# Optimization experiments

Measured on AMD Instinct MI355X. Metric: run time of the kernel, lower is better.

The kernel has to match this reference:

```python
import jax, jax.numpy as jnp
import numpy as np

B, N, M, C, H = 4, 1024, 1024, 768, 12
HD = C // H          # head_dim = in_dim // num_heads = 64
D = H * HD           # inner dim = 768
HID = int(4.0 * C)   # mlp hidden = 3072
EPS = 1e-6
SCALE = HD ** -0.5


def _lin(k, out_d, in_d):
    return jax.random.normal(k, (out_d, in_d), jnp.float32) * 0.02


def setup_inputs() -> dict:
    key = jax.random.key(0)
    ks = jax.random.split(key, 20)
    p = {
        "x": jax.random.normal(ks[0], (B, N, C), jnp.float32),
        "src": jax.random.normal(ks[1], (B, M, C), jnp.float32),
        # self-attention (x stream)
        "w_qkv": _lin(ks[2], 3 * D, C), "w_proj": _lin(ks[3], C, D), "b_proj": jnp.zeros((C,), jnp.float32),
        # self-attention (src stream)
        "w_qkv_s": _lin(ks[4], 3 * D, C), "w_proj_s": _lin(ks[5], C, D), "b_proj_s": jnp.zeros((C,), jnp.float32),
        # bidirectional cross-attention
        "w_qk": _lin(ks[6], 2 * D, C), "w_qk_src": _lin(ks[7], 2 * D, C),
        "w_v": _lin(ks[8], D, C), "w_v_src": _lin(ks[9], D, C),
        "w_cp": _lin(ks[10], C, D), "b_cp": jnp.zeros((C,), jnp.float32),
        "w_cp_src": _lin(ks[11], C, D), "b_cp_src": jnp.zeros((C,), jnp.float32),
        # MLPs
        "mlp1_w": _lin(ks[12], HID, C), "mlp1_b": jnp.zeros((HID,), jnp.float32),
        "mlp2_w": _lin(ks[13], C, HID), "mlp2_b": jnp.zeros((C,), jnp.float32),
        "mlp1s_w": _lin(ks[14], HID, C), "mlp1s_b": jnp.zeros((HID,), jnp.float32),
        "mlp2s_w": _lin(ks[15], C, HID), "mlp2s_b": jnp.zeros((C,), jnp.float32),
    }
    for name in ["ln1", "ln1s", "lnc", "lncs", "ln2", "ln2s"]:
        p[name + "_w"] = jnp.ones((C,), jnp.float32)
        p[name + "_b"] = jnp.zeros((C,), jnp.float32)
    return p


def _ln(x, w, b):
    mu = x.mean(-1, keepdims=True)
    var = ((x - mu) ** 2).mean(-1, keepdims=True)
    return (x - mu) * jax.lax.rsqrt(var + EPS) * w + b


def _heads(t):  # [B,T,(H d)] -> [B,H,T,d]
    b, t_, hd = t.shape
    return t.reshape(b, t_, H, hd // H).transpose(0, 2, 1, 3)


def _merge(t):  # [B,H,T,d] -> [B,T,(H d)]
    b, h, t_, d = t.shape
    return t.transpose(0, 2, 1, 3).reshape(b, t_, h * d)


def _self_attn(x, w_qkv, w_p, b_p):
    b, n, _ = x.shape
    qkv = (x @ w_qkv.T).reshape(b, n, 3, H, HD)
    q = qkv[:, :, 0].transpose(0, 2, 1, 3) * SCALE  # [B,H,N,hd]
    k = qkv[:, :, 1].transpose(0, 2, 1, 3)
    v = qkv[:, :, 2].transpose(0, 2, 1, 3)
    attn = jax.nn.softmax(jnp.einsum('bhnd,bhmd->bhnm', q, k), axis=-1)
    o = _merge(jnp.einsum('bhnm,bhmd->bhnd', attn, v))
    return o @ w_p.T + b_p


def _cross_attn(x, src, w_qk, w_qk_src, w_v, w_v_src, w_cp, b_cp, w_cp_src, b_cp_src):
    # rearrange 'b n (h d) -> b h n d' with h=H on the 2D-wide qk output
    # puts [q_h | k_h] of width 2*HD in the last axis per head
    qk = _heads(x @ w_qk.T)            # [B,H,N,2*hd]
    qk_s = _heads(src @ w_qk_src.T)    # [B,H,M,2*hd]
    v = _heads(x @ w_v.T)              # [B,H,N,hd]
    v_s = _heads(src @ w_v_src.T)      # [B,H,M,hd]
    q, kx = qk[..., :HD] * SCALE, qk[..., HD:] * SCALE
    q_s, k_s = qk_s[..., :HD], qk_s[..., HD:]
    attn = jax.nn.softmax(jnp.einsum('bhnd,bhmd->bhnm', q, q_s), axis=-1)      # x attends to src
    attn_s = jax.nn.softmax(jnp.einsum('bhnd,bhmd->bhmn', kx, k_s), axis=-1)   # src attends to x
    y = _merge(jnp.einsum('bhnm,bhmd->bhnd', attn, v_s)) @ w_cp.T + b_cp
    y_s = _merge(jnp.einsum('bhmn,bhnd->bhmd', attn_s, v)) @ w_cp_src.T + b_cp_src
    return y, y_s


def _mlp(x, w1, b1, w2, b2):
    return jax.nn.gelu(x @ w1.T + b1, approximate=False) @ w2.T + b2


def reference(x, src,
              w_qkv, w_proj, b_proj, w_qkv_s, w_proj_s, b_proj_s,
              w_qk, w_qk_src, w_v, w_v_src, w_cp, b_cp, w_cp_src, b_cp_src,
              mlp1_w, mlp1_b, mlp2_w, mlp2_b, mlp1s_w, mlp1s_b, mlp2s_w, mlp2s_b,
              ln1_w, ln1_b, ln1s_w, ln1s_b, lnc_w, lnc_b, lncs_w, lncs_b,
              ln2_w, ln2_b, ln2s_w, ln2s_b):
    # per-stream self attention (eval: dropout/drop_path identity, no layerscale)
    x = x + _self_attn(_ln(x, ln1_w, ln1_b), w_qkv, w_proj, b_proj)
    src = src + _self_attn(_ln(src, ln1s_w, ln1s_b), w_qkv_s, w_proj_s, b_proj_s)
    # bidirectional cross attention
    y, y_s = _cross_attn(_ln(x, lnc_w, lnc_b), _ln(src, lncs_w, lncs_b),
                         w_qk, w_qk_src, w_v, w_v_src, w_cp, b_cp, w_cp_src, b_cp_src)
    x = x + y
    src = src + y_s
    # per-stream MLP
    x = x + _mlp(_ln(x, ln2_w, ln2_b), mlp1_w, mlp1_b, mlp2_w, mlp2_b)
    src = src + _mlp(_ln(src, ln2s_w, ln2s_b), mlp1s_w, mlp1s_b, mlp2s_w, mlp2s_b)
    return (x, src)
```

## Files before the change

### kernel.cpp

```cpp
#include <hip/hip_runtime.h>
#include <hip/hip_bf16.h>
#include <cmath>


typedef __bf16 bf16_t;
typedef __attribute__((ext_vector_type(8))) __bf16 bf16x8;
typedef __attribute__((ext_vector_type(4))) __bf16 bf16x4;
typedef __attribute__((ext_vector_type(4))) float f32x4;

#define NTOK 4096
#define SCALE_ATTN 0.125f

__device__ __forceinline__ void gload16(const void* g, void* l) {
    __builtin_amdgcn_global_load_lds((const __attribute__((address_space(1))) void*)g,
                                     (__attribute__((address_space(3))) void*)l, 16, 0, 0);
}

struct CvtTab {
    const float* src[14];
    bf16_t* dst[14];
    int n[14];
};
__global__ __launch_bounds__(256) void cvt_all_kernel(CvtTab t) {
    int seg = blockIdx.y;
    int base = blockIdx.x * 2048 + threadIdx.x * 8;
    if (base >= t.n[seg]) return;
    const float* s = t.src[seg];
    float4 a = *(const float4*)(s + base);
    float4 b = *(const float4*)(s + base + 4);
    bf16x8 o;
    o[0] = (bf16_t)a.x; o[1] = (bf16_t)a.y; o[2] = (bf16_t)a.z; o[3] = (bf16_t)a.w;
    o[4] = (bf16_t)b.x; o[5] = (bf16_t)b.y; o[6] = (bf16_t)b.z; o[7] = (bf16_t)b.w;
    *(bf16x8*)(t.dst[seg] + base) = o;
}

__global__ __launch_bounds__(256) void ln_kernel(const float* __restrict__ X,
                                                 const float* __restrict__ w,
                                                 const float* __restrict__ b,
                                                 bf16_t* __restrict__ out) {
    int row = blockIdx.x, t = threadIdx.x;
    const float* x = X + (size_t)row * 768;
    float v0 = x[t], v1 = x[t + 256], v2 = x[t + 512];
    float s = v0 + v1 + v2;
    float s2 = v0 * v0 + v1 * v1 + v2 * v2;
#pragma unroll
    for (int off = 32; off > 0; off >>= 1) {
        s += __shfl_down(s, off);
        s2 += __shfl_down(s2, off);
    }
    __shared__ float as_[4], as2_[4];
    int wave = t >> 6;
    if ((t & 63) == 0) { as_[wave] = s; as2_[wave] = s2; }
    __syncthreads();
    float tot = as_[0] + as_[1] + as_[2] + as_[3];
    float tot2 = as2_[0] + as2_[1] + as2_[2] + as2_[3];
    float mu = tot * (1.f / 768.f);
    float var = tot2 * (1.f / 768.f) - mu * mu;
    float rstd = rsqrtf(var + 1e-6f);
    bf16_t* o = out + (size_t)row * 768;
    o[t]       = (bf16_t)((v0 - mu) * rstd * w[t]       + b[t]);
    o[t + 256] = (bf16_t)((v1 - mu) * rstd * w[t + 256] + b[t + 256]);
    o[t + 512] = (bf16_t)((v2 - mu) * rstd * w[t + 512] + b[t + 512]);
}

__global__ __launch_bounds__(256, 3) void gemm_qkv_kernel(const bf16_t* __restrict__ A,
                                                          const bf16_t* __restrict__ W,
                                                          bf16_t* __restrict__ outQK,
                                                          bf16_t* __restrict__ outVT) {
    __shared__ bf16_t Alds[128 * 64];
    __shared__ bf16_t Blds[128 * 64];
    const int K = 768, GX = 18;
    const int tid = threadIdx.x;
    const int f = blockIdx.x + GX * blockIdx.y;
    const int slot = f >> 3;
    const int bm = (f & 7) * 4 + slot / GX, bn = slot % GX;
    const int lane = tid & 63, wid = tid >> 6;
    const int wm = wid >> 1, wn = wid & 1;
    const int l15 = lane & 15, lh = lane >> 4;
    f32x4 acc[4][4] = {};

    const int lr = lane >> 3;
    const int lc = ((lane & 7) ^ lr) * 8;
    const bf16_t* gA = A + (size_t)(bm * 128 + lr) * K + lc;
    const bf16_t* gB = W + (size_t)(bn * 128 + lr) * K + lc;

    for (int k0 = 0; k0 < K; k0 += 64) {
        __syncthreads();
#pragma unroll
        for (int q = 0; q < 4; ++q) {
            int r0 = (wid * 4 + q) * 8;
            gload16(gA + (size_t)r0 * K + k0, &Alds[r0 * 64]);
            gload16(gB + (size_t)r0 * K + k0, &Blds[r0 * 64]);
        }
        __syncthreads();
#pragma unroll
        for (int kk = 0; kk < 2; ++kk) {
            bf16x8 av[4], bv[4];
#pragma unroll
            for (int i = 0; i < 4; ++i) {
                int rA = wm * 64 + i * 16 + l15;
                int cc = kk * 4 + lh;
                av[i] = *(const bf16x8*)&Alds[rA * 64 + ((cc ^ (rA & 7)) * 8)];
                int rB = wn * 64 + i * 16 + l15;
                bv[i] = *(const bf16x8*)&Blds[rB * 64 + ((cc ^ (rB & 7)) * 8)];
            }
#pragma unroll
            for (int i = 0; i < 4; ++i)
#pragma unroll
                for (int j = 0; j < 4; ++j)
                    acc[i][j] = __builtin_amdgcn_mfma_f32_16x16x32_bf16(av[i], bv[j], acc[i][j], 0, 0, 0);
        }
    }
#pragma unroll
    for (int i = 0; i < 4; ++i) {
        int row0 = bm * 128 + wm * 64 + i * 16 + lh * 4;
#pragma unroll
        for (int j = 0; j < 4; ++j) {
            int col = bn * 128 + wn * 64 + j * 16 + l15;
            if (col < 1536) {
#pragma unroll
                for (int p = 0; p < 4; ++p)
                    outQK[(size_t)(row0 + p) * 1536 + col] = (bf16_t)acc[i][j][p];
            } else {
                bf16x4 pk;
#pragma unroll
                for (int p = 0; p < 4; ++p) pk[p] = (bf16_t)acc[i][j][p];
                *(bf16x4*)&outVT[(size_t)(col - 1536) * NTOK + row0] = pk;
            }
        }
    }
}

__global__ __launch_bounds__(256, 3) void gemm_gelu_kernel(const bf16_t* __restrict__ A,
                                                           const bf16_t* __restrict__ W,
                                                           const float* __restrict__ bias,
                                                           bf16_t* __restrict__ outB) {
    __shared__ bf16_t Alds[128 * 64];
    __shared__ bf16_t Blds[128 * 64];
    const int K = 768, N = 3072, GX = 24;
    const int tid = threadIdx.x;
    const int f = blockIdx.x + GX * blockIdx.y;
    const int slot = f >> 3;
    const int bm = (f & 7) * 4 + slot / GX, bn = slot % GX;
    const int lane = tid & 63, wid = tid >> 6;
    const int wm = wid >> 1, wn = wid & 1;
    const int l15 = lane & 15, lh = lane >> 4;
    f32x4 acc[4][4] = {};

    const int lr = lane >> 3;
    const int lc = ((lane & 7) ^ lr) * 8;
    const bf16_t* gA = A + (size_t)(bm * 128 + lr) * K + lc;
    const bf16_t* gB = W + (size_t)(bn * 128 + lr) * K + lc;

    for (int k0 = 0; k0 < K; k0 += 64) {
        __syncthreads();
#pragma unroll
        for (int q = 0; q < 4; ++q) {
            int r0 = (wid * 4 + q) * 8;
            gload16(gA + (size_t)r0 * K + k0, &Alds[r0 * 64]);
            gload16(gB + (size_t)r0 * K + k0, &Blds[r0 * 64]);
        }
        __syncthreads();
#pragma unroll
        for (int kk = 0; kk < 2; ++kk) {
            bf16x8 av[4], bv[4];
#pragma unroll
            for (int i = 0; i < 4; ++i) {
                int rA = wm * 64 + i * 16 + l15;
                int cc = kk * 4 + lh;
                av[i] = *(const bf16x8*)&Alds[rA * 64 + ((cc ^ (rA & 7)) * 8)];
                int rB = wn * 64 + i * 16 + l15;
                bv[i] = *(const bf16x8*)&Blds[rB * 64 + ((cc ^ (rB & 7)) * 8)];
            }
#pragma unroll
            for (int i = 0; i < 4; ++i)
#pragma unroll
                for (int j = 0; j < 4; ++j)
                    acc[i][j] = __builtin_amdgcn_mfma_f32_16x16x32_bf16(av[i], bv[j], acc[i][j], 0, 0, 0);
        }
    }
#pragma unroll
    for (int i = 0; i < 4; ++i) {
        int row0 = bm * 128 + wm * 64 + i * 16 + lh * 4;
#pragma unroll
        for (int j = 0; j < 4; ++j) {
            int col = bn * 128 + wn * 64 + j * 16 + l15;
            float bv_ = bias[col];
#pragma unroll
            for (int p = 0; p < 4; ++p) {
                float v = acc[i][j][p] + bv_;
                v = 0.5f * v * (1.f + erff(v * 0.70710678118654752f));
                outB[(size_t)(row0 + p) * N + col] = (bf16_t)v;
            }
        }
    }
}

__global__ __launch_bounds__(256, 4) void gemm64_kernel(const bf16_t* __restrict__ A,
                                                        const bf16_t* __restrict__ W,
                                                        const float* __restrict__ bias,
                                                        const float* __restrict__ res,
                                                        float* __restrict__ outF,
                                                        int K) {
    __shared__ bf16_t Alds[128 * 64];
    __shared__ bf16_t Blds[64 * 64];
    const int N = 768, GX = 12;
    const int tid = threadIdx.x;
    const int f = blockIdx.x + GX * blockIdx.y;
    const int slot = f >> 3;
    const int bm = (f & 7) * 4 + slot / GX, bn = slot % GX;
    const int lane = tid & 63, wid = tid >> 6;
    const int l15 = lane & 15, lh = lane >> 4;
    f32x4 acc[2][4] = {};

    const int lr = lane >> 3;
    const int lc = ((lane & 7) ^ lr) * 8;
    const bf16_t* gA = A + (size_t)(bm * 128 + lr) * K + lc;
    const bf16_t* gB = W + (size_t)(bn * 64 + lr) * K + lc;

    for (int k0 = 0; k0 < K; k0 += 64) {
        __syncthreads();
#pragma unroll
        for (int q = 0; q < 4; ++q) {
            int r0 = (wid * 4 + q) * 8;
            gload16(gA + (size_t)r0 * K + k0, &Alds[r0 * 64]);
        }
#pragma unroll
        for (int q = 0; q < 2; ++q) {
            int r0 = (wid * 2 + q) * 8;
            gload16(gB + (size_t)r0 * K + k0, &Blds[r0 * 64]);
        }
        __syncthreads();
#pragma unroll
        for (int kk = 0; kk < 2; ++kk) {
            bf16x8 av[2], bv[4];
#pragma unroll
            for (int i = 0; i < 2; ++i) {
                int rA = wid * 32 + i * 16 + l15;
                int cc = kk * 4 + lh;
                av[i] = *(const bf16x8*)&Alds[rA * 64 + ((cc ^ (rA & 7)) * 8)];
            }
#pragma unroll
            for (int j = 0; j < 4; ++j) {
                int rB = j * 16 + l15;
                int cc = kk * 4 + lh;
                bv[j] = *(const bf16x8*)&Blds[rB * 64 + ((cc ^ (rB & 7)) * 8)];
            }
#pragma unroll
            for (int i = 0; i < 2; ++i)
#pragma unroll
                for (int j = 0; j < 4; ++j)
                    acc[i][j] = __builtin_amdgcn_mfma_f32_16x16x32_bf16(av[i], bv[j], acc[i][j], 0, 0, 0);
        }
    }
#pragma unroll
    for (int i = 0; i < 2; ++i) {
        int row0 = bm * 128 + wid * 32 + i * 16 + lh * 4;
#pragma unroll
        for (int j = 0; j < 4; ++j) {
            int col = bn * 64 + j * 16 + l15;
            float bv_ = bias[col];
#pragma unroll
            for (int p = 0; p < 4; ++p) {
                size_t idx = (size_t)(row0 + p) * N + col;
                outF[idx] = acc[i][j][p] + bv_ + res[idx];
            }
        }
    }
}

__global__ __launch_bounds__(256, 3) void attn_mfma_kernel(const bf16_t* __restrict__ Qp,
                                                           const bf16_t* __restrict__ Kp,
                                                           const bf16_t* __restrict__ VTp,
                                                           bf16_t* __restrict__ Op,
                                                           int ldQ, int ldK,
                                                           int hsQ, int hsK,
                                                           float scale) {
    __shared__ bf16_t Kl[2][64 * 64];
    __shared__ bf16_t Vl[2][64 * 64];
    __shared__ bf16_t Pl[4][16 * 64];
    const int tid = threadIdx.x, lane = tid & 63, w = tid >> 6;
    const int l15 = lane & 15, lh = lane >> 4;
    const int f = blockIdx.x + (blockIdx.y << 4);
    const int slot = f >> 3;
    const int bh = (f & 7) * 6 + (slot >> 4);
    const int q0 = (slot & 15) * 64;
    const int b = bh / 12, h = bh % 12;

    const bf16_t* qptr = Qp + (size_t)(b * 1024 + q0 + w * 16 + l15) * ldQ + h * hsQ + lh * 8;
    bf16x8 qf0 = *(const bf16x8*)qptr;
    bf16x8 qf1 = *(const bf16x8*)(qptr + 32);

    f32x4 oacc[4] = {};
    float m_run[4], l_run[4];
#pragma unroll
    for (int p = 0; p < 4; ++p) { m_run[p] = -1e30f; l_run[p] = 0.f; }

    const int lr = lane >> 3;
    const int lc = ((lane & 7) ^ lr) * 8;
    const bf16_t* kbase = Kp + (size_t)(b * 1024 + lr) * ldK + h * hsK + lc;
    const bf16_t* vbase = VTp + (size_t)(h * 64 + lr) * NTOK + b * 1024 + lc;

    auto stage = [&](int bb, int kt) {
#pragma unroll
        for (int q = 0; q < 2; ++q) {
            int r0 = (w * 2 + q) * 8;
            gload16(kbase + (size_t)(kt + r0) * ldK, &Kl[bb][r0 * 64]);
            gload16(vbase + (size_t)r0 * NTOK + kt, &Vl[bb][r0 * 64]);
        }
    };

    stage(0, 0);
    __syncthreads();

    for (int it = 0; it < 16; ++it) {
        const int cur = it & 1;
        if (it < 15) stage(cur ^ 1, (it + 1) * 64);

        f32x4 s[4] = {};
#pragma unroll
        for (int t = 0; t < 4; ++t) {
            int key = t * 16 + l15;
            bf16x8 kf0 = *(const bf16x8*)&Kl[cur][key * 64 + ((lh ^ (key & 7)) * 8)];
            bf16x8 kf1 = *(const bf16x8*)&Kl[cur][key * 64 + (((4 + lh) ^ (key & 7)) * 8)];
            s[t] = __builtin_amdgcn_mfma_f32_16x16x32_bf16(qf0, kf0, s[t], 0, 0, 0);
            s[t] = __builtin_amdgcn_mfma_f32_16x16x32_bf16(qf1, kf1, s[t], 0, 0, 0);
        }

#pragma unroll
        for (int p = 0; p < 4; ++p) {
            float v0 = s[0][p] * scale, v1 = s[1][p] * scale;
            float v2 = s[2][p] * scale, v3 = s[3][p] * scale;
            float mloc = fmaxf(fmaxf(v0, v1), fmaxf(v2, v3));
#pragma unroll
            for (int off = 1; off < 16; off <<= 1) mloc = fmaxf(mloc, __shfl_xor(mloc, off));
            float mnew = fmaxf(m_run[p], mloc);
            float corr = __expf(m_run[p] - mnew);
            float p0 = __expf(v0 - mnew), p1 = __expf(v1 - mnew);
            float p2 = __expf(v2 - mnew), p3 = __expf(v3 - mnew);
            float ps = p0 + p1 + p2 + p3;
#pragma unroll
            for (int off = 1; off < 16; off <<= 1) ps += __shfl_xor(ps, off);
            l_run[p] = l_run[p] * corr + ps;
            m_run[p] = mnew;
            oacc[0][p] *= corr; oacc[1][p] *= corr; oacc[2][p] *= corr; oacc[3][p] *= corr;
            int r = lh * 4 + p;
            bf16_t* pr = &Pl[w][r * 64];
            int cb = l15 >> 3, ce = l15 & 7, rs = r & 7;
            pr[((0 + cb) ^ rs) * 8 + ce] = (bf16_t)p0;
            pr[((2 + cb) ^ rs) * 8 + ce] = (bf16_t)p1;
            pr[((4 + cb) ^ rs) * 8 + ce] = (bf16_t)p2;
            pr[((6 + cb) ^ rs) * 8 + ce] = (bf16_t)p3;
        }

#pragma unroll
        for (int kk = 0; kk < 2; ++kk) {
            bf16x8 pf = *(const bf16x8*)&Pl[w][l15 * 64 + (((kk * 4 + lh) ^ (l15 & 7)) * 8)];
#pragma unroll
            for (int dt = 0; dt < 4; ++dt) {
                int d = dt * 16 + l15;
                bf16x8 vf = *(const bf16x8*)&Vl[cur][d * 64 + (((kk * 4 + lh) ^ (d & 7)) * 8)];
                oacc[dt] = __builtin_amdgcn_mfma_f32_16x16x32_bf16(pf, vf, oacc[dt], 0, 0, 0);
            }
        }

        __syncthreads();
    }

    float inv[4];
#pragma unroll
    for (int p = 0; p < 4; ++p) inv[p] = 1.f / l_run[p];
#pragma unroll
    for (int dt = 0; dt < 4; ++dt) {
#pragma unroll
        for (int p = 0; p < 4; ++p) {
            int row = q0 + w * 16 + lh * 4 + p;
            int col = h * 64 + dt * 16 + l15;
            Op[(size_t)(b * 1024 + row) * 768 + col] = (bf16_t)(oacc[dt][p] * inv[p]);
        }
    }
}

extern "C" void kernel_launch(void* const* d_in, const int* in_sizes, int n_in,
                              void* d_out, int out_size, void* d_ws, size_t ws_size,
                              hipStream_t stream) {
    const float* x_in   = (const float*)d_in[0];
    const float* src_in = (const float*)d_in[1];
    const float* b_proj   = (const float*)d_in[4];
    const float* b_proj_s = (const float*)d_in[7];
    const float* b_cp     = (const float*)d_in[13];
    const float* b_cp_s   = (const float*)d_in[15];
    const float* mlp1_b   = (const float*)d_in[17];
    const float* mlp2_b   = (const float*)d_in[19];
    const float* mlp1s_b  = (const float*)d_in[21];
    const float* mlp2s_b  = (const float*)d_in[23];
    const float* ln1_w  = (const float*)d_in[24];
    const float* ln1_b  = (const float*)d_in[25];
    const float* ln1s_w = (const float*)d_in[26];
    const float* ln1s_b = (const float*)d_in[27];
    const float* lnc_w  = (const float*)d_in[28];
    const float* lnc_b  = (const float*)d_in[29];
    const float* lncs_w = (const float*)d_in[30];
    const float* lncs_b = (const float*)d_in[31];
    const float* ln2_w  = (const float*)d_in[32];
    const float* ln2_b  = (const float*)d_in[33];
    const float* ln2s_w = (const float*)d_in[34];
    const float* ln2s_b = (const float*)d_in[35];

    char* ws = (char*)d_ws;
    size_t off = 0;
    auto alloc = [&](size_t bytes) -> void* {
        void* p = ws + off;
        off = (off + bytes + 255) & ~(size_t)255;
        return p;
    };

    bf16_t* bw_qkv_x = (bf16_t*)alloc((size_t)2304 * 768 * 2);
    bf16_t* bw_proj_x = (bf16_t*)alloc((size_t)768 * 768 * 2);
    bf16_t* bw_qkv_s = (bf16_t*)alloc((size_t)2304 * 768 * 2);
    bf16_t* bw_proj_s = (bf16_t*)alloc((size_t)768 * 768 * 2);
    bf16_t* bw_cx    = (bf16_t*)alloc((size_t)2304 * 768 * 2);
    bf16_t* bw_cs    = (bf16_t*)alloc((size_t)2304 * 768 * 2);
    bf16_t* bw_cp    = (bf16_t*)alloc((size_t)768 * 768 * 2);
    bf16_t* bw_cp_s  = (bf16_t*)alloc((size_t)768 * 768 * 2);
    bf16_t* bw_mlp1  = (bf16_t*)alloc((size_t)3072 * 768 * 2);
    bf16_t* bw_mlp2  = (bf16_t*)alloc((size_t)768 * 3072 * 2);
    bf16_t* bw_mlp1s = (bf16_t*)alloc((size_t)3072 * 768 * 2);
    bf16_t* bw_mlp2s = (bf16_t*)alloc((size_t)768 * 3072 * 2);

    bf16_t* arena = (bf16_t*)alloc((size_t)NTOK * 3072 * 2 * 2);
    bf16_t* LN_A = (bf16_t*)alloc((size_t)NTOK * 768 * 2);
    bf16_t* LN_B = (bf16_t*)alloc((size_t)NTOK * 768 * 2);
    bf16_t* O_A  = (bf16_t*)alloc((size_t)NTOK * 768 * 2);
    bf16_t* O_B  = (bf16_t*)alloc((size_t)NTOK * 768 * 2);

    float* Xst = (float*)d_out;
    float* Sst = (float*)d_out + (size_t)NTOK * 768;

    bf16_t* SQK = arena;
    bf16_t* VTs = arena + (size_t)NTOK * 1536;
    bf16_t* QKx = arena;
    bf16_t* QKs = arena + (size_t)NTOK * 1536;
    bf16_t* VxT = arena + (size_t)NTOK * 3072;
    bf16_t* VsT = arena + (size_t)NTOK * 3072 + (size_t)768 * NTOK;
    bf16_t* H_A = arena;
    bf16_t* H_B = arena + (size_t)NTOK * 3072;

    CvtTab tab;
    const float* csrc[14] = {(const float*)d_in[2], (const float*)d_in[3],
                             (const float*)d_in[5], (const float*)d_in[6],
                             (const float*)d_in[8], (const float*)d_in[10],
                             (const float*)d_in[9], (const float*)d_in[11],
                             (const float*)d_in[12], (const float*)d_in[14],
                             (const float*)d_in[16], (const float*)d_in[18],
                             (const float*)d_in[20], (const float*)d_in[22]};
    bf16_t* cdst[14] = {bw_qkv_x, bw_proj_x, bw_qkv_s, bw_proj_s,
                        bw_cx, bw_cx + (size_t)1536 * 768,
                        bw_cs, bw_cs + (size_t)1536 * 768,
                        bw_cp, bw_cp_s, bw_mlp1, bw_mlp2, bw_mlp1s, bw_mlp2s};
    int cn[14] = {2304 * 768, 768 * 768, 2304 * 768, 768 * 768,
                  1536 * 768, 768 * 768, 1536 * 768, 768 * 768,
                  768 * 768, 768 * 768, 3072 * 768, 768 * 3072, 3072 * 768, 768 * 3072};
    for (int i = 0; i < 14; ++i) { tab.src[i] = csrc[i]; tab.dst[i] = cdst[i]; tab.n[i] = cn[i]; }
    cvt_all_kernel<<<dim3(1152, 14), 256, 0, stream>>>(tab);

    const dim3 blk(256);
    const dim3 qkv_grid(18, 32);
    const dim3 g64_grid(12, 32);
    const dim3 gelu_grid(24, 32);
    const dim3 attn_grid(16, 48);

    ln_kernel<<<NTOK, blk, 0, stream>>>(x_in, ln1_w, ln1_b, LN_A);
    gemm_qkv_kernel<<<qkv_grid, blk, 0, stream>>>(LN_A, bw_qkv_x, SQK, VTs);
    attn_mfma_kernel<<<attn_grid, blk, 0, stream>>>(SQK, SQK + 768, VTs, O_A, 1536, 1536, 64, 64, SCALE_ATTN);
    gemm64_kernel<<<g64_grid, blk, 0, stream>>>(O_A, bw_proj_x, b_proj, x_in, Xst, 768);

    ln_kernel<<<NTOK, blk, 0, stream>>>(src_in, ln1s_w, ln1s_b, LN_A);
    gemm_qkv_kernel<<<qkv_grid, blk, 0, stream>>>(LN_A, bw_qkv_s, SQK, VTs);
    attn_mfma_kernel<<<attn_grid, blk, 0, stream>>>(SQK, SQK + 768, VTs, O_A, 1536, 1536, 64, 64, SCALE_ATTN);
    gemm64_kernel<<<g64_grid, blk, 0, stream>>>(O_A, bw_proj_s, b_proj_s, src_in, Sst, 768);

    ln_kernel<<<NTOK, blk, 0, stream>>>(Xst, lnc_w, lnc_b, LN_A);
    ln_kernel<<<NTOK, blk, 0, stream>>>(Sst, lncs_w, lncs_b, LN_B);
    gemm_qkv_kernel<<<qkv_grid, blk, 0, stream>>>(LN_A, bw_cx, QKx, VxT);
    gemm_qkv_kernel<<<qkv_grid, blk, 0, stream>>>(LN_B, bw_cs, QKs, VsT);
    attn_mfma_kernel<<<attn_grid, blk, 0, stream>>>(QKx, QKs, VsT, O_A, 1536, 1536, 128, 128, SCALE_ATTN);
    attn_mfma_kernel<<<attn_grid, blk, 0, stream>>>(QKs + 64, QKx + 64, VxT, O_B, 1536, 1536, 128, 128, SCALE_ATTN);
    gemm64_kernel<<<g64_grid, blk, 0, stream>>>(O_A, bw_cp, b_cp, Xst, Xst, 768);
    gemm64_kernel<<<g64_grid, blk, 0, stream>>>(O_B, bw_cp_s, b_cp_s, Sst, Sst, 768);

    ln_kernel<<<NTOK, blk, 0, stream>>>(Xst, ln2_w, ln2_b, LN_A);
    ln_kernel<<<NTOK, blk, 0, stream>>>(Sst, ln2s_w, ln2s_b, LN_B);
    gemm_gelu_kernel<<<gelu_grid, blk, 0, stream>>>(LN_A, bw_mlp1, mlp1_b, H_A);
    gemm_gelu_kernel<<<gelu_grid, blk, 0, stream>>>(LN_B, bw_mlp1s, mlp1s_b, H_B);
    gemm64_kernel<<<g64_grid, blk, 0, stream>>>(H_A, bw_mlp2, mlp2_b, Xst, Xst, 3072);
    gemm64_kernel<<<g64_grid, blk, 0, stream>>>(H_B, bw_mlp2s, mlp2s_b, Sst, Sst, 3072);
}
```

Baseline: 676.8 us.

## Double-buffer 64x64 projection GEMM tiles and transpose attention MFMA operands

The residual projection GEMM moves from 128x64 single-buffered tiles to 64x64 tiles with a double-buffered LDS prefetch and a 2x2 warp layout, which doubles the grid. This is meant to overlap global loads with MFMA work and give more blocks for occupancy. The attention kernel swaps the MFMA operand order so each lane owns one query row. That turns the per-row softmax reductions into two cross-lane shuffles instead of four-step butterflies across four rows, and lets P and the output be stored as packed bf16x4 vectors. The cost is less reuse per block in the GEMM, and correctness depends on the transposed accumulator layout mapping.

```diff
diff --git a/kernel.cpp b/kernel.cpp
--- a/kernel.cpp
+++ b/kernel.cpp
@@ -202,63 +202,65 @@
                                                         const float* __restrict__ res,
                                                         float* __restrict__ outF,
                                                         int K) {
-    __shared__ bf16_t Alds[128 * 64];
-    __shared__ bf16_t Blds[64 * 64];
+    __shared__ bf16_t Alds[2][64 * 64];
+    __shared__ bf16_t Blds[2][64 * 64];
     const int N = 768, GX = 12;
     const int tid = threadIdx.x;
     const int f = blockIdx.x + GX * blockIdx.y;
     const int slot = f >> 3;
-    const int bm = (f & 7) * 4 + slot / GX, bn = slot % GX;
+    const int bm = (f & 7) * 8 + slot / GX;
+    const int bn = slot % GX;
     const int lane = tid & 63, wid = tid >> 6;
+    const int wm = wid >> 1, wn = wid & 1;
     const int l15 = lane & 15, lh = lane >> 4;
-    f32x4 acc[2][4] = {};
+    f32x4 acc[2][2] = {};
 
     const int lr = lane >> 3;
     const int lc = ((lane & 7) ^ lr) * 8;
-    const bf16_t* gA = A + (size_t)(bm * 128 + lr) * K + lc;
+    const bf16_t* gA = A + (size_t)(bm * 64 + lr) * K + lc;
     const bf16_t* gB = W + (size_t)(bn * 64 + lr) * K + lc;
 
-    for (int k0 = 0; k0 < K; k0 += 64) {
-        __syncthreads();
-#pragma unroll
-        for (int q = 0; q < 4; ++q) {
-            int r0 = (wid * 4 + q) * 8;
-            gload16(gA + (size_t)r0 * K + k0, &Alds[r0 * 64]);
-        }
+    auto stage = [&](int bb, int k0) {
 #pragma unroll
         for (int q = 0; q < 2; ++q) {
             int r0 = (wid * 2 + q) * 8;
-            gload16(gB + (size_t)r0 * K + k0, &Blds[r0 * 64]);
+            gload16(gA + (size_t)r0 * K + k0, &Alds[bb][r0 * 64]);
+            gload16(gB + (size_t)r0 * K + k0, &Blds[bb][r0 * 64]);
+        }
+    };
+
+    const int NT = K >> 6;
+    stage(0, 0);
+    __syncthreads();
+
+    for (int it = 0; it < NT; ++it) {
+        const int cur = it & 1;
+        if (it + 1 < NT) stage(cur ^ 1, (it + 1) * 64);
+#pragma unroll
+        for (int kk = 0; kk < 2; ++kk) {
+            bf16x8 av[2], bv[2];
+            int cc = kk * 4 + lh;
+#pragma unroll
+            for (int i = 0; i < 2; ++i) {
+                int rA = wm * 32 + i * 16 + l15;
+                av[i] = *(const bf16x8*)&Alds[cur][rA * 64 + ((cc ^ (rA & 7)) * 8)];
+                int rB = wn * 32 + i * 16 + l15;
+                bv[i] = *(const bf16x8*)&Blds[cur][rB * 64 + ((cc ^ (rB & 7)) * 8)];
+            }
+#pragma unroll
+            for (int i = 0; i < 2; ++i)
+#pragma unroll
+                for (int j = 0; j < 2; ++j)
+                    acc[i][j] = __builtin_amdgcn_mfma_f32_16x16x32_bf16(av[i], bv[j], acc[i][j], 0, 0, 0);
         }
         __syncthreads();
-#pragma unroll
-        for (int kk = 0; kk < 2; ++kk) {
-            bf16x8 av[2], bv[4];
-#pragma unroll
-            for (int i = 0; i < 2; ++i) {
-                int rA = wid * 32 + i * 16 + l15;
-                int cc = kk * 4 + lh;
-                av[i] = *(const bf16x8*)&Alds[rA * 64 + ((cc ^ (rA & 7)) * 8)];
-            }
-#pragma unroll
-            for (int j = 0; j < 4; ++j) {
-                int rB = j * 16 + l15;
-                int cc = kk * 4 + lh;
-                bv[j] = *(const bf16x8*)&Blds[rB * 64 + ((cc ^ (rB & 7)) * 8)];
-            }
-#pragma unroll
-            for (int i = 0; i < 2; ++i)
-#pragma unroll
-                for (int j = 0; j < 4; ++j)
-                    acc[i][j] = __builtin_amdgcn_mfma_f32_16x16x32_bf16(av[i], bv[j], acc[i][j], 0, 0, 0);
-        }
     }
 #pragma unroll
     for (int i = 0; i < 2; ++i) {
-        int row0 = bm * 128 + wid * 32 + i * 16 + lh * 4;
-#pragma unroll
-        for (int j = 0; j < 4; ++j) {
-            int col = bn * 64 + j * 16 + l15;
+        int row0 = bm * 64 + wm * 32 + i * 16 + lh * 4;
+#pragma unroll
+        for (int j = 0; j < 2; ++j) {
+            int col = bn * 64 + wn * 32 + j * 16 + l15;
             float bv_ = bias[col];
 #pragma unroll
             for (int p = 0; p < 4; ++p) {
@@ -292,9 +294,7 @@
     bf16x8 qf1 = *(const bf16x8*)(qptr + 32);
 
     f32x4 oacc[4] = {};
-    float m_run[4], l_run[4];
-#pragma unroll
-    for (int p = 0; p < 4; ++p) { m_run[p] = -1e30f; l_run[p] = 0.f; }
+    float m_run = -1e30f, l_run = 0.f;
 
     const int lr = lane >> 3;
     const int lc = ((lane & 7) ^ lr) * 8;
@@ -323,61 +323,67 @@
             int key = t * 16 + l15;
             bf16x8 kf0 = *(const bf16x8*)&Kl[cur][key * 64 + ((lh ^ (key & 7)) * 8)];
             bf16x8 kf1 = *(const bf16x8*)&Kl[cur][key * 64 + (((4 + lh) ^ (key & 7)) * 8)];
-            s[t] = __builtin_amdgcn_mfma_f32_16x16x32_bf16(qf0, kf0, s[t], 0, 0, 0);
-            s[t] = __builtin_amdgcn_mfma_f32_16x16x32_bf16(qf1, kf1, s[t], 0, 0, 0);
-        }
-
-#pragma unroll
-        for (int p = 0; p < 4; ++p) {
-            float v0 = s[0][p] * scale, v1 = s[1][p] * scale;
-            float v2 = s[2][p] * scale, v3 = s[3][p] * scale;
-            float mloc = fmaxf(fmaxf(v0, v1), fmaxf(v2, v3));
-#pragma unroll
-            for (int off = 1; off < 16; off <<= 1) mloc = fmaxf(mloc, __shfl_xor(mloc, off));
-            float mnew = fmaxf(m_run[p], mloc);
-            float corr = __expf(m_run[p] - mnew);
-            float p0 = __expf(v0 - mnew), p1 = __expf(v1 - mnew);
-            float p2 = __expf(v2 - mnew), p3 = __expf(v3 - mnew);
-            float ps = p0 + p1 + p2 + p3;
-#pragma unroll
-            for (int off = 1; off < 16; off <<= 1) ps += __shfl_xor(ps, off);
-            l_run[p] = l_run[p] * corr + ps;
-            m_run[p] = mnew;
-            oacc[0][p] *= corr; oacc[1][p] *= corr; oacc[2][p] *= corr; oacc[3][p] *= corr;
-            int r = lh * 4 + p;
-            bf16_t* pr = &Pl[w][r * 64];
-            int cb = l15 >> 3, ce = l15 & 7, rs = r & 7;
-            pr[((0 + cb) ^ rs) * 8 + ce] = (bf16_t)p0;
-            pr[((2 + cb) ^ rs) * 8 + ce] = (bf16_t)p1;
-            pr[((4 + cb) ^ rs) * 8 + ce] = (bf16_t)p2;
-            pr[((6 + cb) ^ rs) * 8 + ce] = (bf16_t)p3;
-        }
+            s[t] = __builtin_amdgcn_mfma_f32_16x16x32_bf16(kf0, qf0, s[t], 0, 0, 0);
+            s[t] = __builtin_amdgcn_mfma_f32_16x16x32_bf16(kf1, qf1, s[t], 0, 0, 0);
+        }
+
+        float v[4][4];
+        float mx = -1e30f;
+#pragma unroll
+        for (int t = 0; t < 4; ++t)
+#pragma unroll
+            for (int p = 0; p < 4; ++p) {
+                v[t][p] = s[t][p] * scale;
+                mx = fmaxf(mx, v[t][p]);
+            }
+        mx = fmaxf(mx, __shfl_xor(mx, 16));
+        mx = fmaxf(mx, __shfl_xor(mx, 32));
+        float mnew = fmaxf(m_run, mx);
+        float corr = __expf(m_run - mnew);
+        m_run = mnew;
+        float ps = 0.f;
+        const int rs = l15 & 7;
+        bf16_t* prow = &Pl[w][l15 * 64];
+#pragma unroll
+        for (int t = 0; t < 4; ++t) {
+            bf16x4 pk;
+#pragma unroll
+            for (int p = 0; p < 4; ++p) {
+                float ev = __expf(v[t][p] - mnew);
+                ps += ev;
+                pk[p] = (bf16_t)ev;
+            }
+            int c = 2 * t + (lh >> 1);
+            *(bf16x4*)&prow[((c ^ rs) * 8) + (lh & 1) * 4] = pk;
+        }
+        ps += __shfl_xor(ps, 16);
+        ps += __shfl_xor(ps, 32);
+        l_run = l_run * corr + ps;
+#pragma unroll
+        for (int dt = 0; dt < 4; ++dt) oacc[dt] *= corr;
 
 #pragma unroll
         for (int kk = 0; kk < 2; ++kk) {
-            bf16x8 pf = *(const bf16x8*)&Pl[w][l15 * 64 + (((kk * 4 + lh) ^ (l15 & 7)) * 8)];
+            bf16x8 pf = *(const bf16x8*)&prow[(((kk * 4 + lh) ^ rs) * 8)];
 #pragma unroll
             for (int dt = 0; dt < 4; ++dt) {
                 int d = dt * 16 + l15;
                 bf16x8 vf = *(const bf16x8*)&Vl[cur][d * 64 + (((kk * 4 + lh) ^ (d & 7)) * 8)];
-                oacc[dt] = __builtin_amdgcn_mfma_f32_16x16x32_bf16(pf, vf, oacc[dt], 0, 0, 0);
+                oacc[dt] = __builtin_amdgcn_mfma_f32_16x16x32_bf16(vf, pf, oacc[dt], 0, 0, 0);
             }
         }
 
         __syncthreads();
     }
 
-    float inv[4];
-#pragma unroll
-    for (int p = 0; p < 4; ++p) inv[p] = 1.f / l_run[p];
+    float inv = 1.f / l_run;
+    bf16_t* orow = Op + (size_t)(b * 1024 + q0 + w * 16 + l15) * 768 + h * 64;
 #pragma unroll
     for (int dt = 0; dt < 4; ++dt) {
-#pragma unroll
-        for (int p = 0; p < 4; ++p) {
-            int row = q0 + w * 16 + lh * 4 + p;
-            int col = h * 64 + dt * 16 + l15;
-            Op[(size_t)(b * 1024 + row) * 768 + col] = (bf16_t)(oacc[dt][p] * inv[p]);
-        }
+        bf16x4 pk;
+#pragma unroll
+        for (int p = 0; p < 4; ++p) pk[p] = (bf16_t)(oacc[dt][p] * inv);
+        *(bf16x4*)&orow[dt * 16 + lh * 4] = pk;
     }
 }
 
@@ -466,7 +472,7 @@
 
     const dim3 blk(256);
     const dim3 qkv_grid(18, 32);
-    const dim3 g64_grid(12, 32);
+    const dim3 g64_grid(12, 64);
     const dim3 gelu_grid(24, 32);
     const dim3 attn_grid(16, 48);
 
```

New measurement: 609.8 us. 9.9% less time.
